# Performance work log

Hardware: AMD Instinct MI355X
Metric: run time of the kernel (lower is better)

## Reference

```python
import jax, jax.numpy as jnp
import numpy as np

# Hard-coded 36-node detector graph from the source (1-indexed), 220 directed edges.
E_SRC = [1,2,3,4,5,6,7,8,9,10,11,12,13,14,15,16,17,18,19,20,21,22,23,24,25,26,27,28,29,30,31,32,33,34,35,36,4,3,8,7,19,20,15,16,35,36,31,32,11,12,11,11,11,12,12,12,6,5,25,26,28,25,9,9,9,10,10,10,1,2,3,4,5,6,7,8,9,10,11,12,13,14,15,16,17,18,17,18,19,20,16,15,31,32,36,35,3,4,7,8,6,5,25,28,14,9,12,11,1,4,2,3,4,1,6,7,8,5,10,11,12,9,14,15,16,13,18,19,20,17,22,23,24,21,26,27,28,25,30,31,32,29,34,35,36,33,33,34,1,2,14,13,30,29,23,22,21,24,22,21,36,33,4,31,30,15,27,28,18,17,10,9,14,19,18,5,8,1,19,20,21,22,23,24,25,26,27,28,29,30,31,32,33,34,35,36,25,26,13,14,30,29,24,21,23,22,33,34,1,2,28,27,10,9,12,15,22,21,11,10]
E_DST = [2,3,4,1,6,7,8,5,10,11,12,9,14,15,16,13,18,19,20,17,22,23,24,21,26,27,28,25,30,31,32,29,34,35,36,33,33,34,1,2,14,13,30,29,23,22,21,24,22,21,36,33,4,31,30,15,27,28,18,17,10,9,14,19,18,5,8,1,19,20,21,22,23,24,25,26,27,28,29,30,31,32,33,34,35,36,25,26,13,14,30,29,24,21,23,22,33,34,1,2,28,27,10,9,12,15,22,21,11,10,1,2,3,4,5,6,7,8,9,10,11,12,13,14,15,16,17,18,19,20,21,22,23,24,25,26,27,28,29,30,31,32,33,34,35,36,4,3,8,7,19,20,15,16,35,36,31,32,11,12,11,11,11,12,12,12,6,5,25,26,28,25,9,9,9,10,10,10,1,2,3,4,5,6,7,8,9,10,11,12,13,14,15,16,17,18,17,18,19,20,16,15,31,32,36,35,3,4,7,8,6,5,25,28,14,9,12,11,1,4]

B = 20000   # graphs per batch
P = 36      # nodes per graph
N = B * P


def setup_inputs() -> dict:
    key = jax.random.key(0)
    ks = jax.random.split(key, 12)
    src = np.asarray(E_SRC, np.int32) - 1
    dst = np.asarray(E_DST, np.int32) - 1
    offs = (np.arange(B, dtype=np.int32) * P)[:, None]
    edge_index = jnp.asarray(np.stack([(src[None, :] + offs).reshape(-1),
                                       (dst[None, :] + offs).reshape(-1)]))  # [2, B*220]
    batch_index = jnp.asarray(np.repeat(np.arange(B, dtype=np.int32), P))  # [N]
    x = jax.random.normal(ks[0], (N, 2), jnp.float32)
    pos = jax.random.normal(ks[1], (N, 3), jnp.float32)  # unused by forward (faithful to source)

    def lin_w(k, fi, fo):
        s = 1.0 / np.sqrt(fi)
        return jax.random.uniform(k, (fi, fo), jnp.float32, -s, s)

    def lin_b(k, fo):
        return jax.random.uniform(k, (fo,), jnp.float32, -0.05, 0.05)

    return {
        "x": x, "edge_index": edge_index, "pos": pos, "batch_index": batch_index,
        "W0": lin_w(ks[2], 2, 4),   "b0": lin_b(ks[3], 4),
        "W1": lin_w(ks[4], 4, 12),  "b1": lin_b(ks[5], 12),
        "W2": lin_w(ks[6], 12, 16), "b2": lin_b(ks[7], 16),
        "W3": lin_w(ks[8], 16, 32), "b3": lin_b(ks[9], 32),
        "Wfc": lin_w(ks[10], 64, 7), "bfc": lin_b(ks[11], 7),
    }


def reference(x, edge_index, pos, batch_index, W0, b0, W1, b1, W2, b2, W3, b3, Wfc, bfc):
    del pos  # present in the torch signature but unused
    src, dst = edge_index[0], edge_index[1]
    n = x.shape[0]
    # GCN symmetric normalization with self-loops: deg = 1 + in-degree
    deg = jax.ops.segment_sum(jnp.ones(src.shape, x.dtype), dst, num_segments=n) + 1.0
    inv = deg ** -0.5
    enorm = inv[src] * inv[dst]   # edge norm
    snorm = inv * inv             # self-loop norm (deg^-1)

    def gcn_conv(h, W, b):
        h = h @ W  # [n, fo]
        agg = jax.ops.segment_sum(h[src] * enorm[:, None], dst, num_segments=n)
        return agg + h * snorm[:, None] + b

    h = jax.nn.relu(gcn_conv(x, W0, b0))
    h = jax.nn.relu(gcn_conv(h, W1, b1))
    # dropout(0.2) is identity in eval mode
    h = jax.nn.relu(gcn_conv(h, W2, b2))
    h = jax.nn.relu(gcn_conv(h, W3, b3))

    gmp = jax.ops.segment_max(h, batch_index, num_segments=B)
    counts = jax.ops.segment_sum(jnp.ones((n,), h.dtype), batch_index, num_segments=B)
    gap = jax.ops.segment_sum(h, batch_index, num_segments=B) / counts[:, None]
    hidden = jnp.concatenate([gmp, gap], axis=1)  # [B, 64]
    out = jax.nn.relu(hidden @ Wfc + bfc)         # [B, 7]
    return (out, hidden)
```

## Files before the change

kernel.cpp:

```cpp
#include <hip/hip_runtime.h>

typedef __attribute__((ext_vector_type(2))) float f32x2;
typedef __attribute__((ext_vector_type(4))) float f32x4;

#define NGRAPH 20000
#define GPB 7
#define STRIDE 36
#define SB (STRIDE * 4)

static __constant__ int c_indeg[36] = {
    7,5,5,7,6,5,5,6,9,9,9,9,5,7,7,5,5,6,6,5,7,7,5,5,7,5,5,7,5,6,6,5,6,5,5,6
};
static __constant__ signed char c_adj[36][9] = {
    {3,7,9,6,1,18,10,0,0},      {0,6,7,2,19,0,0,0,0},
    {1,3,33,32,20,0,0,0,0},     {2,10,0,32,21,33,9,0,0},
    {7,9,5,27,22,26,0,0,0},     {4,6,26,23,27,0,0,0,0},
    {5,7,1,24,0,0,0,0,0},       {6,9,4,0,25,1,0,0,0},
    {11,24,27,9,13,18,17,26,14},{8,27,24,3,10,4,7,0,27},
    {9,0,11,21,35,32,3,28,20},  {10,13,8,20,30,29,14,29,21},
    {15,19,18,13,30,0,0,0,0},   {12,18,8,19,14,31,11,0,0},
    {13,11,8,15,29,32,28,0,0},  {14,12,28,33,29,0,0,0,0},
    {19,25,17,34,24,0,0,0,0},   {16,24,8,18,35,25,0,0,0},
    {17,8,0,19,13,12,0,0,0},    {18,1,16,12,13,0,0,0,0},
    {23,30,11,2,31,10,21,0,0},  {20,35,10,3,34,11,22,0,0},
    {21,34,4,35,23,0,0,0,0},    {22,31,5,30,20,0,0,0,0},
    {27,6,16,25,17,8,9,0,0},    {24,7,17,26,16,0,0,0,0},
    {25,5,8,27,4,0,0,0,0},      {26,4,9,5,24,9,8,0,0},
    {31,15,10,14,29,0,0,0,0},   {28,14,11,11,15,30,0,0,0},
    {29,11,12,31,20,23,0,0,0},  {30,13,28,23,20,0,0,0,0},
    {35,3,10,14,2,33,0,0,0},    {32,2,15,3,34,0,0,0,0},
    {33,16,35,22,21,0,0,0,0},   {34,10,17,32,21,22,0,0,0},
};
static __constant__ float c_inv[36] = {
    0.35355339f,0.40824829f,0.40824829f,0.35355339f,0.37796447f,0.40824829f,
    0.40824829f,0.37796447f,0.31622777f,0.31622777f,0.31622777f,0.31622777f,
    0.40824829f,0.35355339f,0.35355339f,0.40824829f,0.40824829f,0.37796447f,
    0.37796447f,0.40824829f,0.35355339f,0.35355339f,0.40824829f,0.40824829f,
    0.35355339f,0.40824829f,0.40824829f,0.35355339f,0.40824829f,0.37796447f,
    0.37796447f,0.40824829f,0.37796447f,0.40824829f,0.40824829f,0.37796447f,
};
#define A_ 0.35355339f
#define B_ 0.40824829f
#define C_ 0.37796447f
#define D_ 0.31622777f
static __constant__ float c_ninv[36][9] = {
    {A_,C_,D_,B_,B_,C_,D_,0,0}, {A_,B_,C_,B_,B_,0,0,0,0},
    {B_,A_,B_,C_,A_,0,0,0,0},   {B_,D_,A_,C_,A_,B_,D_,0,0},
    {C_,D_,B_,A_,B_,B_,0,0,0},  {C_,B_,B_,B_,A_,0,0,0,0},
    {B_,C_,B_,A_,A_,0,0,0,0},   {B_,D_,C_,A_,B_,B_,0,0,0},
    {D_,A_,A_,D_,A_,C_,C_,B_,A_},{D_,A_,A_,A_,D_,C_,C_,A_,A_},
    {D_,A_,D_,A_,C_,C_,A_,B_,A_},{D_,A_,D_,A_,C_,C_,A_,C_,A_},
    {B_,B_,C_,A_,C_,0,0,0,0},   {B_,C_,D_,B_,A_,B_,D_,0,0},
    {A_,D_,D_,B_,C_,C_,B_,0,0}, {A_,B_,B_,B_,C_,0,0,0,0},
    {B_,B_,C_,B_,A_,0,0,0,0},   {B_,A_,D_,C_,C_,B_,0,0,0},
    {C_,D_,A_,B_,A_,B_,0,0,0},  {C_,B_,B_,B_,A_,0,0,0,0},
    {B_,C_,D_,B_,B_,D_,A_,0,0}, {A_,C_,D_,A_,B_,D_,B_,0,0},
    {A_,B_,C_,C_,B_,0,0,0,0},   {B_,B_,B_,C_,A_,0,0,0,0},
    {A_,B_,B_,B_,C_,D_,D_,0,0}, {A_,C_,C_,B_,B_,0,0,0,0},
    {B_,B_,D_,A_,C_,0,0,0,0},   {B_,C_,D_,B_,A_,D_,D_,0,0},
    {B_,B_,D_,A_,C_,0,0,0,0},   {B_,A_,D_,D_,B_,C_,0,0,0},
    {C_,D_,B_,B_,A_,B_,0,0,0},  {C_,A_,B_,B_,A_,0,0,0,0},
    {C_,A_,D_,A_,B_,B_,0,0,0},  {C_,B_,B_,A_,B_,0,0,0,0},
    {B_,B_,C_,B_,A_,0,0,0,0},   {B_,D_,C_,C_,A_,B_,0,0,0},
};

static __device__ __forceinline__ f32x2 relu2(f32x2 v) {
    return __builtin_elementwise_max(v, (f32x2){0.f, 0.f});
}

extern "C" __global__ __launch_bounds__(256, 4)
void gcn_fused(const float* __restrict__ x,
               const float* __restrict__ W0, const float* __restrict__ b0,
               const float* __restrict__ W1, const float* __restrict__ b1,
               const float* __restrict__ W2, const float* __restrict__ b2,
               const float* __restrict__ W3, const float* __restrict__ b3,
               const float* __restrict__ Wfc, const float* __restrict__ bfc,
               float* __restrict__ out)
{
    __shared__ float L[GPB * 36 * STRIDE];

    const int t = threadIdx.x;
    const int g = t / 36;
    const int v = t - g * 36;
    const bool act = (g < GPB);
    const int gq = act ? g : GPB - 1;
    const int vc = act ? v : 0;
    const int G  = blockIdx.x * GPB + g;
    const int Gc = (act && G < NGRAPH) ? G : 0;

    const int nd = c_indeg[vc];
    const float inv_v = c_inv[vc];
    int nb[9], aoff[9];
    {
        const unsigned char* ar = (const unsigned char*)&c_adj[vc][0];
        const unsigned int w0 = *(const unsigned int*)(ar);
        const unsigned int w1 = *(const unsigned int*)(ar + 4);
        const unsigned int w2 = *(const unsigned int*)(ar + 8);
#pragma unroll
        for (int k = 0; k < 4; ++k) nb[k] = (int)((w0 >> (8 * k)) & 0xff);
#pragma unroll
        for (int k = 0; k < 4; ++k) nb[4 + k] = (int)((w1 >> (8 * k)) & 0xff);
        nb[8] = (int)(w2 & 0xff);
#pragma unroll
        for (int k = 0; k < 9; ++k) aoff[k] = (gq * 36 + nb[k]) * SB;
    }
    float* srow = &L[(gq * 36 + vc) * STRIDE];
    const char* Lb = (const char*)L;

    f32x2 h0a, h0b;
    {
        const float2* x2 = (const float2*)x;
        const int xb = Gc * 36;
        const float2 xs = x2[xb + vc];
        f32x2 acc = {xs.x * inv_v, xs.y * inv_v};
        const float* nr = &c_ninv[vc][0];
#pragma unroll
        for (int k = 0; k < 5; ++k) {
            const float2 xu = x2[xb + nb[k]];
            const float w = nr[k];
            acc.x = fmaf(w, xu.x, acc.x); acc.y = fmaf(w, xu.y, acc.y);
        }
        if (nd > 5) { const float2 xu = x2[xb + nb[5]]; const float w = nr[5];
            acc.x = fmaf(w, xu.x, acc.x); acc.y = fmaf(w, xu.y, acc.y); }
        if (nd > 6) { const float2 xu = x2[xb + nb[6]]; const float w = nr[6];
            acc.x = fmaf(w, xu.x, acc.x); acc.y = fmaf(w, xu.y, acc.y); }
        if (nd > 7) {
            const float2 xu7 = x2[xb + nb[7]]; const float w7 = nr[7];
            acc.x = fmaf(w7, xu7.x, acc.x); acc.y = fmaf(w7, xu7.y, acc.y);
            const float2 xu8 = x2[xb + nb[8]]; const float w8 = nr[8];
            acc.x = fmaf(w8, xu8.x, acc.x); acc.y = fmaf(w8, xu8.y, acc.y);
        }
        const float a0 = acc.x * inv_v, a1 = acc.y * inv_v;
        const f32x2 a0v = {a0, a0}, a1v = {a1, a1};
        const f32x2* W0v = (const f32x2*)W0;
        const f32x2* b0v = (const f32x2*)b0;
        h0a = relu2(__builtin_elementwise_fma(a0v, W0v[0],
                    __builtin_elementwise_fma(a1v, W0v[2], b0v[0])));
        h0b = relu2(__builtin_elementwise_fma(a0v, W0v[1],
                    __builtin_elementwise_fma(a1v, W0v[3], b0v[1])));
    }

    f32x2 h1[6];
    {
        const f32x2 iv = {inv_v, inv_v};
        const f32x2 s0 = h0a * iv, s1 = h0b * iv;
        if (act) *(f32x4*)&srow[0] = (f32x4){s0.x, s0.y, s1.x, s1.y};
        __syncthreads();
        f32x4 c = {s0.x, s0.y, s1.x, s1.y};
#pragma unroll
        for (int k = 0; k < 5; ++k) c += *(const f32x4*)(Lb + aoff[k]);
        if (nd > 5) c += *(const f32x4*)(Lb + aoff[5]);
        if (nd > 6) c += *(const f32x4*)(Lb + aoff[6]);
        if (nd > 7) { c += *(const f32x4*)(Lb + aoff[7]);
                      c += *(const f32x4*)(Lb + aoff[8]); }
        float a[4];
#pragma unroll
        for (int i = 0; i < 4; ++i) a[i] = c[i] * inv_v;
        f32x2 z[6];
        const f32x2* b1v = (const f32x2*)b1;
#pragma unroll
        for (int j = 0; j < 6; ++j) z[j] = b1v[j];
        const f32x2* W1v = (const f32x2*)W1;
#pragma unroll
        for (int i = 0; i < 4; ++i) {
            const f32x2 av = {a[i], a[i]};
#pragma unroll
            for (int j = 0; j < 6; ++j)
                z[j] = __builtin_elementwise_fma(av, W1v[i * 6 + j], z[j]);
        }
#pragma unroll
        for (int j = 0; j < 6; ++j) h1[j] = relu2(z[j]);
    }

    f32x2 h2[8];
    {
        const f32x2 iv = {inv_v, inv_v};
        f32x2 s[6];
#pragma unroll
        for (int j = 0; j < 6; ++j) s[j] = h1[j] * iv;
        if (act) {
            *(f32x4*)&srow[4]  = (f32x4){s[0].x, s[0].y, s[1].x, s[1].y};
            *(f32x4*)&srow[8]  = (f32x4){s[2].x, s[2].y, s[3].x, s[3].y};
            *(f32x4*)&srow[12] = (f32x4){s[4].x, s[4].y, s[5].x, s[5].y};
        }
        __syncthreads();
        f32x4 c0 = {s[0].x, s[0].y, s[1].x, s[1].y};
        f32x4 c1 = {s[2].x, s[2].y, s[3].x, s[3].y};
        f32x4 c2 = {s[4].x, s[4].y, s[5].x, s[5].y};
#pragma unroll
        for (int k = 0; k < 5; ++k) {
            const char* base = Lb + aoff[k] + 16;
            c0 += *(const f32x4*)(base);
            c1 += *(const f32x4*)(base + 16);
            c2 += *(const f32x4*)(base + 32);
        }
        if (nd > 5) { const char* base = Lb + aoff[5] + 16;
            c0 += *(const f32x4*)(base); c1 += *(const f32x4*)(base + 16);
            c2 += *(const f32x4*)(base + 32); }
        if (nd > 6) { const char* base = Lb + aoff[6] + 16;
            c0 += *(const f32x4*)(base); c1 += *(const f32x4*)(base + 16);
            c2 += *(const f32x4*)(base + 32); }
        if (nd > 7) {
            const char* ba = Lb + aoff[7] + 16;
            c0 += *(const f32x4*)(ba); c1 += *(const f32x4*)(ba + 16);
            c2 += *(const f32x4*)(ba + 32);
            const char* bb = Lb + aoff[8] + 16;
            c0 += *(const f32x4*)(bb); c1 += *(const f32x4*)(bb + 16);
            c2 += *(const f32x4*)(bb + 32);
        }
        float a[12];
#pragma unroll
        for (int i = 0; i < 4; ++i) {
            a[i] = c0[i] * inv_v; a[4 + i] = c1[i] * inv_v; a[8 + i] = c2[i] * inv_v;
        }
        f32x2 z[8];
        const f32x2* b2v = (const f32x2*)b2;
#pragma unroll
        for (int j = 0; j < 8; ++j) z[j] = b2v[j];
        const f32x2* W2v = (const f32x2*)W2;
#pragma unroll
        for (int i = 0; i < 12; ++i) {
            const f32x2 av = {a[i], a[i]};
#pragma unroll
            for (int j = 0; j < 8; ++j)
                z[j] = __builtin_elementwise_fma(av, W2v[i * 8 + j], z[j]);
        }
#pragma unroll
        for (int j = 0; j < 8; ++j) h2[j] = relu2(z[j]);
    }

    f32x2 h3[16];
    {
        const f32x2 iv = {inv_v, inv_v};
        f32x2 s[8];
#pragma unroll
        for (int j = 0; j < 8; ++j) s[j] = h2[j] * iv;
        if (act) {
#pragma unroll
            for (int q = 0; q < 4; ++q)
                *(f32x4*)&srow[16 + q * 4] =
                    (f32x4){s[2*q].x, s[2*q].y, s[2*q+1].x, s[2*q+1].y};
        }
        __syncthreads();
        f32x4 c0 = {s[0].x, s[0].y, s[1].x, s[1].y};
        f32x4 c1 = {s[2].x, s[2].y, s[3].x, s[3].y};
        f32x4 c2 = {s[4].x, s[4].y, s[5].x, s[5].y};
        f32x4 c3 = {s[6].x, s[6].y, s[7].x, s[7].y};
#pragma unroll
        for (int k = 0; k < 5; ++k) {
            const char* base = Lb + aoff[k] + 64;
            c0 += *(const f32x4*)(base);      c1 += *(const f32x4*)(base + 16);
            c2 += *(const f32x4*)(base + 32); c3 += *(const f32x4*)(base + 48);
        }
        if (nd > 5) { const char* base = Lb + aoff[5] + 64;
            c0 += *(const f32x4*)(base);      c1 += *(const f32x4*)(base + 16);
            c2 += *(const f32x4*)(base + 32); c3 += *(const f32x4*)(base + 48); }
        if (nd > 6) { const char* base = Lb + aoff[6] + 64;
            c0 += *(const f32x4*)(base);      c1 += *(const f32x4*)(base + 16);
            c2 += *(const f32x4*)(base + 32); c3 += *(const f32x4*)(base + 48); }
        if (nd > 7) {
            const char* ba = Lb + aoff[7] + 64;
            c0 += *(const f32x4*)(ba);      c1 += *(const f32x4*)(ba + 16);
            c2 += *(const f32x4*)(ba + 32); c3 += *(const f32x4*)(ba + 48);
            const char* bb = Lb + aoff[8] + 64;
            c0 += *(const f32x4*)(bb);      c1 += *(const f32x4*)(bb + 16);
            c2 += *(const f32x4*)(bb + 32); c3 += *(const f32x4*)(bb + 48);
        }
        float a[16];
#pragma unroll
        for (int i = 0; i < 4; ++i) {
            a[i] = c0[i] * inv_v;      a[4 + i] = c1[i] * inv_v;
            a[8 + i] = c2[i] * inv_v;  a[12 + i] = c3[i] * inv_v;
        }
        f32x2 z[16];
        const f32x2* b3v = (const f32x2*)b3;
#pragma unroll
        for (int j = 0; j < 16; ++j) z[j] = b3v[j];
        const f32x2* W3v = (const f32x2*)W3;
#pragma unroll
        for (int i = 0; i < 16; ++i) {
            const f32x2 av = {a[i], a[i]};
#pragma unroll
            for (int j = 0; j < 16; ++j)
                z[j] = __builtin_elementwise_fma(av, W3v[i * 16 + j], z[j]);
        }
#pragma unroll
        for (int j = 0; j < 16; ++j) h3[j] = relu2(z[j]);
    }

    if (act) {
#pragma unroll
        for (int q = 0; q < 4; ++q)
            *(f32x4*)&srow[q * 4] =
                (f32x4){h3[2*q].x, h3[2*q].y, h3[2*q+1].x, h3[2*q+1].y};
    }
    __syncthreads();
    if (act) {
#pragma unroll
        for (int q = 0; q < 4; ++q)
            *(f32x4*)&srow[16 + q * 4] =
                (f32x4){h3[8+2*q].x, h3[8+2*q].y, h3[9+2*q].x, h3[9+2*q].y};
    }
    __syncthreads();

    if (t < GPB * 32) {
        const int pg = t >> 5, pf = t & 31;
        const int PG = blockIdx.x * GPB + pg;
        const float* col = &L[(pg * 36) * STRIDE + pf];
        float mx = -1e30f, sm = 0.f;
#pragma unroll
        for (int u = 0; u < 18; ++u) {
            const float v0 = col[0], v1 = col[STRIDE];
            mx = fmaxf(mx, fmaxf(v0, v1)); sm += v0 + v1;
            col += 2 * STRIDE;
        }
        const float gap = sm * (1.0f / 36.0f);
        if (PG < NGRAPH) {
            float* ho = out + (size_t)NGRAPH * 7 + (size_t)PG * 64;
            ho[pf] = mx; ho[32 + pf] = gap;
        }
        float p[7];
        const float* wr0 = Wfc + pf * 7;
        const float* wr1 = Wfc + (32 + pf) * 7;
#pragma unroll
        for (int o = 0; o < 7; ++o)
            p[o] = fmaf(mx, wr0[o], gap * wr1[o]);
#pragma unroll
        for (int m = 16; m >= 1; m >>= 1) {
#pragma unroll
            for (int o = 0; o < 7; ++o)
                p[o] += __shfl_xor(p[o], m, 32);
        }
        if (pf < 7 && PG < NGRAPH) {
            float w = p[0];
            w = (pf == 1) ? p[1] : w;
            w = (pf == 2) ? p[2] : w;
            w = (pf == 3) ? p[3] : w;
            w = (pf == 4) ? p[4] : w;
            w = (pf == 5) ? p[5] : w;
            w = (pf == 6) ? p[6] : w;
            out[(size_t)PG * 7 + pf] = fmaxf(w + bfc[pf], 0.f);
        }
    }
}

extern "C" void kernel_launch(void* const* d_in, const int* in_sizes, int n_in,
                              void* d_out, int out_size, void* d_ws, size_t ws_size,
                              hipStream_t stream) {
    (void)in_sizes; (void)n_in; (void)d_ws; (void)ws_size; (void)out_size;
    const float* x   = (const float*)d_in[0];
    const float* W0  = (const float*)d_in[4];
    const float* b0  = (const float*)d_in[5];
    const float* W1  = (const float*)d_in[6];
    const float* b1  = (const float*)d_in[7];
    const float* W2  = (const float*)d_in[8];
    const float* b2  = (const float*)d_in[9];
    const float* W3  = (const float*)d_in[10];
    const float* b3  = (const float*)d_in[11];
    const float* Wfc = (const float*)d_in[12];
    const float* bfc = (const float*)d_in[13];
    float* out = (float*)d_out;

    const int nblocks = (NGRAPH + GPB - 1) / GPB;
    hipLaunchKernelGGL(gcn_fused, dim3(nblocks), dim3(256), 0, stream,
                       x, W0, b0, W1, b1, W2, b2, W3, b3, Wfc, bfc, out);
}
```

Measured before the change: 36.40 us.

## Store layer 1-2 activations as fp16 in LDS and gather layer-0 inputs via LDS

Layer-0 neighbour features are now staged in shared memory and gathered from there instead of through repeated global loads. Layers 1 and 2 write unscaled activations to LDS as fp16 and apply the per-neighbour normalisation weights during the gather, which halves LDS traffic for those layers. The final h3 store split and the pooling loop are reshuffled to fit the new layout. This adds an extra barrier and fp16 rounding error in the intermediate activations, and the pooling reads are less unrolled.

```diff
diff --git a/kernel.cpp b/kernel.cpp
--- a/kernel.cpp
+++ b/kernel.cpp
@@ -2,6 +2,9 @@
 
 typedef __attribute__((ext_vector_type(2))) float f32x2;
 typedef __attribute__((ext_vector_type(4))) float f32x4;
+typedef _Float16 f16;
+typedef __attribute__((ext_vector_type(4))) _Float16 f16x4;
+typedef __attribute__((ext_vector_type(8))) _Float16 f16x8;
 
 #define NGRAPH 20000
 #define GPB 7
@@ -90,47 +93,29 @@
 
     const int nd = c_indeg[vc];
     const float inv_v = c_inv[vc];
-    int nb[9], aoff[9];
-    {
-        const unsigned char* ar = (const unsigned char*)&c_adj[vc][0];
-        const unsigned int w0 = *(const unsigned int*)(ar);
-        const unsigned int w1 = *(const unsigned int*)(ar + 4);
-        const unsigned int w2 = *(const unsigned int*)(ar + 8);
-#pragma unroll
-        for (int k = 0; k < 4; ++k) nb[k] = (int)((w0 >> (8 * k)) & 0xff);
-#pragma unroll
-        for (int k = 0; k < 4; ++k) nb[4 + k] = (int)((w1 >> (8 * k)) & 0xff);
-        nb[8] = (int)(w2 & 0xff);
-#pragma unroll
-        for (int k = 0; k < 9; ++k) aoff[k] = (gq * 36 + nb[k]) * SB;
-    }
+    const float* nr = &c_ninv[vc][0];
+    int aoff[9];
+#pragma unroll
+    for (int k = 0; k < 9; ++k)
+        aoff[k] = (gq * 36 + (int)c_adj[vc][k]) * SB;
     float* srow = &L[(gq * 36 + vc) * STRIDE];
+    char* srowb = (char*)srow;
     const char* Lb = (const char*)L;
 
     f32x2 h0a, h0b;
     {
-        const float2* x2 = (const float2*)x;
-        const int xb = Gc * 36;
-        const float2 xs = x2[xb + vc];
-        f32x2 acc = {xs.x * inv_v, xs.y * inv_v};
-        const float* nr = &c_ninv[vc][0];
-#pragma unroll
-        for (int k = 0; k < 5; ++k) {
-            const float2 xu = x2[xb + nb[k]];
-            const float w = nr[k];
-            acc.x = fmaf(w, xu.x, acc.x); acc.y = fmaf(w, xu.y, acc.y);
-        }
-        if (nd > 5) { const float2 xu = x2[xb + nb[5]]; const float w = nr[5];
-            acc.x = fmaf(w, xu.x, acc.x); acc.y = fmaf(w, xu.y, acc.y); }
-        if (nd > 6) { const float2 xu = x2[xb + nb[6]]; const float w = nr[6];
-            acc.x = fmaf(w, xu.x, acc.x); acc.y = fmaf(w, xu.y, acc.y); }
-        if (nd > 7) {
-            const float2 xu7 = x2[xb + nb[7]]; const float w7 = nr[7];
-            acc.x = fmaf(w7, xu7.x, acc.x); acc.y = fmaf(w7, xu7.y, acc.y);
-            const float2 xu8 = x2[xb + nb[8]]; const float w8 = nr[8];
-            acc.x = fmaf(w8, xu8.x, acc.x); acc.y = fmaf(w8, xu8.y, acc.y);
-        }
-        const float a0 = acc.x * inv_v, a1 = acc.y * inv_v;
+        const float2 xv = ((const float2*)x)[(size_t)Gc * 36 + vc];
+        const float s0 = xv.x * inv_v, s1 = xv.y * inv_v;
+        if (act) { srow[32] = s0; srow[33] = s1; }
+        __syncthreads();
+        f32x2 c = {s0, s1};
+#pragma unroll
+        for (int k = 0; k < 5; ++k) c += *(const f32x2*)(Lb + aoff[k] + 128);
+        if (nd > 5) c += *(const f32x2*)(Lb + aoff[5] + 128);
+        if (nd > 6) c += *(const f32x2*)(Lb + aoff[6] + 128);
+        if (nd > 7) { c += *(const f32x2*)(Lb + aoff[7] + 128);
+                      c += *(const f32x2*)(Lb + aoff[8] + 128); }
+        const float a0 = c.x * inv_v, a1 = c.y * inv_v;
         const f32x2 a0v = {a0, a0}, a1v = {a1, a1};
         const f32x2* W0v = (const f32x2*)W0;
         const f32x2* b0v = (const f32x2*)b0;
@@ -174,45 +159,47 @@
 
     f32x2 h2[8];
     {
-        const f32x2 iv = {inv_v, inv_v};
-        f32x2 s[6];
-#pragma unroll
-        for (int j = 0; j < 6; ++j) s[j] = h1[j] * iv;
         if (act) {
-            *(f32x4*)&srow[4]  = (f32x4){s[0].x, s[0].y, s[1].x, s[1].y};
-            *(f32x4*)&srow[8]  = (f32x4){s[2].x, s[2].y, s[3].x, s[3].y};
-            *(f32x4*)&srow[12] = (f32x4){s[4].x, s[4].y, s[5].x, s[5].y};
+            f16x8 wlo; f16x4 whi;
+#pragma unroll
+            for (int j = 0; j < 4; ++j) {
+                wlo[2*j]   = (f16)h1[j].x;
+                wlo[2*j+1] = (f16)h1[j].y;
+            }
+#pragma unroll
+            for (int j = 0; j < 2; ++j) {
+                whi[2*j]   = (f16)h1[4+j].x;
+                whi[2*j+1] = (f16)h1[4+j].y;
+            }
+            *(f16x8*)(srowb + 16) = wlo;
+            *(f16x4*)(srowb + 32) = whi;
         }
         __syncthreads();
-        f32x4 c0 = {s[0].x, s[0].y, s[1].x, s[1].y};
-        f32x4 c1 = {s[2].x, s[2].y, s[3].x, s[3].y};
-        f32x4 c2 = {s[4].x, s[4].y, s[5].x, s[5].y};
-#pragma unroll
-        for (int k = 0; k < 5; ++k) {
-            const char* base = Lb + aoff[k] + 16;
-            c0 += *(const f32x4*)(base);
-            c1 += *(const f32x4*)(base + 16);
-            c2 += *(const f32x4*)(base + 32);
-        }
-        if (nd > 5) { const char* base = Lb + aoff[5] + 16;
-            c0 += *(const f32x4*)(base); c1 += *(const f32x4*)(base + 16);
-            c2 += *(const f32x4*)(base + 32); }
-        if (nd > 6) { const char* base = Lb + aoff[6] + 16;
-            c0 += *(const f32x4*)(base); c1 += *(const f32x4*)(base + 16);
-            c2 += *(const f32x4*)(base + 32); }
-        if (nd > 7) {
-            const char* ba = Lb + aoff[7] + 16;
-            c0 += *(const f32x4*)(ba); c1 += *(const f32x4*)(ba + 16);
-            c2 += *(const f32x4*)(ba + 32);
-            const char* bb = Lb + aoff[8] + 16;
-            c0 += *(const f32x4*)(bb); c1 += *(const f32x4*)(bb + 16);
-            c2 += *(const f32x4*)(bb + 32);
+        float c[12];
+#pragma unroll
+        for (int j = 0; j < 6; ++j) {
+            c[2*j]   = h1[j].x * inv_v;
+            c[2*j+1] = h1[j].y * inv_v;
+        }
+#pragma unroll
+        for (int k = 0; k < 9; ++k) {
+            if (k >= 5) {
+                if (k == 5 && nd <= 5) break;
+                if (k == 6 && nd <= 6) break;
+                if (k == 7 && nd <= 7) break;
+            }
+            const char* base = Lb + aoff[k];
+            const f16x8 lo = *(const f16x8*)(base + 16);
+            const f16x4 hi = *(const f16x4*)(base + 32);
+            const float w = nr[k];
+#pragma unroll
+            for (int i = 0; i < 8; ++i) c[i]     = fmaf((float)lo[i], w, c[i]);
+#pragma unroll
+            for (int i = 0; i < 4; ++i) c[8 + i] = fmaf((float)hi[i], w, c[8 + i]);
         }
         float a[12];
 #pragma unroll
-        for (int i = 0; i < 4; ++i) {
-            a[i] = c0[i] * inv_v; a[4 + i] = c1[i] * inv_v; a[8 + i] = c2[i] * inv_v;
-        }
+        for (int i = 0; i < 12; ++i) a[i] = c[i] * inv_v;
         f32x2 z[8];
         const f32x2* b2v = (const f32x2*)b2;
 #pragma unroll
@@ -231,47 +218,44 @@
 
     f32x2 h3[16];
     {
-        const f32x2 iv = {inv_v, inv_v};
-        f32x2 s[8];
-#pragma unroll
-        for (int j = 0; j < 8; ++j) s[j] = h2[j] * iv;
         if (act) {
-#pragma unroll
-            for (int q = 0; q < 4; ++q)
-                *(f32x4*)&srow[16 + q * 4] =
-                    (f32x4){s[2*q].x, s[2*q].y, s[2*q+1].x, s[2*q+1].y};
+            f16x8 wlo, whi;
+#pragma unroll
+            for (int j = 0; j < 4; ++j) {
+                wlo[2*j]   = (f16)h2[j].x;
+                wlo[2*j+1] = (f16)h2[j].y;
+                whi[2*j]   = (f16)h2[4+j].x;
+                whi[2*j+1] = (f16)h2[4+j].y;
+            }
+            *(f16x8*)(srowb + 48) = wlo;
+            *(f16x8*)(srowb + 64) = whi;
         }
         __syncthreads();
-        f32x4 c0 = {s[0].x, s[0].y, s[1].x, s[1].y};
-        f32x4 c1 = {s[2].x, s[2].y, s[3].x, s[3].y};
-        f32x4 c2 = {s[4].x, s[4].y, s[5].x, s[5].y};
-        f32x4 c3 = {s[6].x, s[6].y, s[7].x, s[7].y};
-#pragma unroll
-        for (int k = 0; k < 5; ++k) {
-            const char* base = Lb + aoff[k] + 64;
-            c0 += *(const f32x4*)(base);      c1 += *(const f32x4*)(base + 16);
-            c2 += *(const f32x4*)(base + 32); c3 += *(const f32x4*)(base + 48);
-        }
-        if (nd > 5) { const char* base = Lb + aoff[5] + 64;
-            c0 += *(const f32x4*)(base);      c1 += *(const f32x4*)(base + 16);
-            c2 += *(const f32x4*)(base + 32); c3 += *(const f32x4*)(base + 48); }
-        if (nd > 6) { const char* base = Lb + aoff[6] + 64;
-            c0 += *(const f32x4*)(base);      c1 += *(const f32x4*)(base + 16);
-            c2 += *(const f32x4*)(base + 32); c3 += *(const f32x4*)(base + 48); }
-        if (nd > 7) {
-            const char* ba = Lb + aoff[7] + 64;
-            c0 += *(const f32x4*)(ba);      c1 += *(const f32x4*)(ba + 16);
-            c2 += *(const f32x4*)(ba + 32); c3 += *(const f32x4*)(ba + 48);
-            const char* bb = Lb + aoff[8] + 64;
-            c0 += *(const f32x4*)(bb);      c1 += *(const f32x4*)(bb + 16);
-            c2 += *(const f32x4*)(bb + 32); c3 += *(const f32x4*)(bb + 48);
+        float c[16];
+#pragma unroll
+        for (int j = 0; j < 8; ++j) {
+            c[2*j]   = h2[j].x * inv_v;
+            c[2*j+1] = h2[j].y * inv_v;
+        }
+#pragma unroll
+        for (int k = 0; k < 9; ++k) {
+            if (k >= 5) {
+                if (k == 5 && nd <= 5) break;
+                if (k == 6 && nd <= 6) break;
+                if (k == 7 && nd <= 7) break;
+            }
+            const char* base = Lb + aoff[k];
+            const f16x8 lo = *(const f16x8*)(base + 48);
+            const f16x8 hi = *(const f16x8*)(base + 64);
+            const float w = nr[k];
+#pragma unroll
+            for (int i = 0; i < 8; ++i) c[i]     = fmaf((float)lo[i], w, c[i]);
+#pragma unroll
+            for (int i = 0; i < 8; ++i) c[8 + i] = fmaf((float)hi[i], w, c[8 + i]);
         }
         float a[16];
 #pragma unroll
-        for (int i = 0; i < 4; ++i) {
-            a[i] = c0[i] * inv_v;      a[4 + i] = c1[i] * inv_v;
-            a[8 + i] = c2[i] * inv_v;  a[12 + i] = c3[i] * inv_v;
-        }
+        for (int i = 0; i < 16; ++i) a[i] = c[i] * inv_v;
         f32x2 z[16];
         const f32x2* b3v = (const f32x2*)b3;
 #pragma unroll
@@ -289,17 +273,16 @@
     }
 
     if (act) {
-#pragma unroll
-        for (int q = 0; q < 4; ++q)
-            *(f32x4*)&srow[q * 4] =
-                (f32x4){h3[2*q].x, h3[2*q].y, h3[2*q+1].x, h3[2*q+1].y};
+        *(f32x4*)&srow[0] = (f32x4){h3[0].x, h3[0].y, h3[1].x, h3[1].y};
+        *(f32x4*)&srow[4] = (f32x4){h3[2].x, h3[2].y, h3[3].x, h3[3].y};
+        *(f32x4*)&srow[8] = (f32x4){h3[4].x, h3[4].y, h3[5].x, h3[5].y};
     }
     __syncthreads();
     if (act) {
 #pragma unroll
-        for (int q = 0; q < 4; ++q)
-            *(f32x4*)&srow[16 + q * 4] =
-                (f32x4){h3[8+2*q].x, h3[8+2*q].y, h3[9+2*q].x, h3[9+2*q].y};
+        for (int q = 0; q < 5; ++q)
+            *(f32x4*)&srow[12 + q * 4] =
+                (f32x4){h3[6+2*q].x, h3[6+2*q].y, h3[7+2*q].x, h3[7+2*q].y};
     }
     __syncthreads();
 
@@ -309,10 +292,9 @@
         const float* col = &L[(pg * 36) * STRIDE + pf];
         float mx = -1e30f, sm = 0.f;
 #pragma unroll
-        for (int u = 0; u < 18; ++u) {
-            const float v0 = col[0], v1 = col[STRIDE];
-            mx = fmaxf(mx, fmaxf(v0, v1)); sm += v0 + v1;
-            col += 2 * STRIDE;
+        for (int u = 0; u < 36; ++u) {
+            const float val = col[u * STRIDE];
+            mx = fmaxf(mx, val); sm += val;
         }
         const float gap = sm * (1.0f / 36.0f);
         if (PG < NGRAPH) {
```

After: 36.64 us. About the same (+0.7%).
